# Optimization experiments

Hardware: AMD Instinct MI355X
Metric: run time of the kernel (lower is better)

The kernel has to match this reference:

```python
import jax, jax.numpy as jnp
import numpy as np
import math

B, L, D, H = 4, 2048, 512, 8
DH = D // H
FACTOR = 5.0
EPS = 1e-9
# static top-k count: min(L_q, max(1, int(factor * log(L_q + eps))))
K_TOP = min(L, max(1, int(FACTOR * math.log(L + EPS))))  # = 38
SCALE = 1.0 / math.sqrt(DH)


def setup_inputs() -> dict:
    key = jax.random.key(0)
    ks = jax.random.split(key, 9)
    s = 1.0 / math.sqrt(D)
    return {
        "x": jax.random.normal(ks[0], (B, L, D), jnp.float32),
        "Wq": jax.random.normal(ks[1], (D, D), jnp.float32) * s,
        "bq": jax.random.normal(ks[2], (D,), jnp.float32) * 0.01,
        "Wk": jax.random.normal(ks[3], (D, D), jnp.float32) * s,
        "bk": jax.random.normal(ks[4], (D,), jnp.float32) * 0.01,
        "Wv": jax.random.normal(ks[5], (D, D), jnp.float32) * s,
        "bv": jax.random.normal(ks[6], (D,), jnp.float32) * 0.01,
        "Wo": jax.random.normal(ks[7], (D, D), jnp.float32) * s,
        "bo": jax.random.normal(ks[8], (D,), jnp.float32) * 0.01,
    }


def _project(x, W, b):
    # [B, L, D] -> [B*H, L, DH]
    y = x @ W + b
    return y.reshape(B, L, H, DH).transpose(0, 2, 1, 3).reshape(B * H, L, DH)


def reference(x, Wq, bq, Wk, bk, Wv, bv, Wo, bo):
    Q = _project(x, Wq, bq)
    K = _project(x, Wk, bk)
    V = _project(x, Wv, bv)

    # full scores for sparsity measure: [BH, L, L]
    scores = jnp.einsum('bqd,bkd->bqk', Q, K) * SCALE
    M = scores.max(axis=-1) - scores.mean(axis=-1)  # [BH, L]
    _, top_idx = jax.lax.top_k(M, K_TOP)            # [BH, K_TOP]

    # gather sparse queries, sparse attention
    Q_sparse = jnp.take_along_axis(Q, top_idx[:, :, None], axis=1)  # [BH, K_TOP, DH]
    scores_sparse = jnp.einsum('bqd,bkd->bqk', Q_sparse, K) * SCALE
    attn = jax.nn.softmax(scores_sparse, axis=-1)
    context_sparse = attn @ V                                        # [BH, K_TOP, DH]

    # mean-filled context, scatter sparse results back
    V_mean = V.mean(axis=1, keepdims=True)                           # [BH, 1, DH]
    context = jnp.broadcast_to(V_mean, (B * H, L, DH))
    bidx = jnp.arange(B * H)[:, None]
    context = context.at[bidx, top_idx, :].set(context_sparse)

    # merge heads, output projection
    out = context.reshape(B, H, L, DH).transpose(0, 2, 1, 3).reshape(B, L, D)
    return out @ Wo + bo
```

## Files before the change

### kernel.cpp

```cpp
#include <hip/hip_runtime.h>

#define BB   4
#define LL   2048
#define DD   512
#define HH   8
#define DH   64
#define BH   32
#define KTOP 38
#define NCAND 64
#define SCALEF 0.125f

#define NSP  16
#define CHK  128
#define QPAD 48
#define SCS  132
#define VST  66

typedef __attribute__((ext_vector_type(8))) short bf16x8;
typedef __attribute__((ext_vector_type(8))) unsigned short ushort8;
typedef __attribute__((ext_vector_type(4))) float f32x4;

__device__ __forceinline__ ushort f32_to_bf16_rn(float x) {
    unsigned u = __float_as_uint(x);
    u += 0x7fffu + ((u >> 16) & 1u);
    return (ushort)(u >> 16);
}
__device__ __forceinline__ float bf16_to_f32(ushort h) {
    return __uint_as_float(((unsigned)h) << 16);
}
__device__ __forceinline__ unsigned int pack_hl(float x) {
    ushort h = f32_to_bf16_rn(x);
    ushort l = f32_to_bf16_rn(x - bf16_to_f32(h));
    return ((unsigned int)l << 16) | (unsigned int)h;
}

__global__ __launch_bounds__(256) void split_x(const float* __restrict__ X,
                                               ushort* __restrict__ XH,
                                               ushort* __restrict__ XL) {
    const size_t c = (size_t)blockIdx.x * 256 + threadIdx.x;
    const float4 v = *(const float4*)&X[c * 4];
    ushort4 h, l;
    h.x = f32_to_bf16_rn(v.x); l.x = f32_to_bf16_rn(v.x - bf16_to_f32(h.x));
    h.y = f32_to_bf16_rn(v.y); l.y = f32_to_bf16_rn(v.y - bf16_to_f32(h.y));
    h.z = f32_to_bf16_rn(v.z); l.z = f32_to_bf16_rn(v.z - bf16_to_f32(h.z));
    h.w = f32_to_bf16_rn(v.w); l.w = f32_to_bf16_rn(v.w - bf16_to_f32(h.w));
    *(ushort4*)&XH[c * 4] = h;
    *(ushort4*)&XL[c * 4] = l;
}

__global__ __launch_bounds__(256) void split_wT(const float* __restrict__ W0,
                                                const float* __restrict__ W1,
                                                const float* __restrict__ W2,
                                                const float* __restrict__ W3,
                                                ushort* __restrict__ WTH,
                                                ushort* __restrict__ WTL) {
    __shared__ float tile[32][33];
    const int z = blockIdx.z;
    const float* W = (z == 0) ? W0 : (z == 1) ? W1 : (z == 2) ? W2 : W3;
    ushort* oh = WTH + (size_t)z * DD * DD;
    ushort* ol = WTL + (size_t)z * DD * DD;
    const int n0 = blockIdx.x * 32, k0 = blockIdx.y * 32;
    const int t = threadIdx.x;
    const int r = t >> 5, c = t & 31;
    #pragma unroll
    for (int i = 0; i < 4; i++)
        tile[r + i * 8][c] = W[(size_t)(k0 + r + i * 8) * DD + n0 + c];
    __syncthreads();
    #pragma unroll
    for (int i = 0; i < 4; i++) {
        int row = r + i * 8;
        float v = tile[c][row];
        ushort h = f32_to_bf16_rn(v);
        oh[(size_t)(n0 + row) * DD + k0 + c] = h;
        ol[(size_t)(n0 + row) * DD + k0 + c] = f32_to_bf16_rn(v - bf16_to_f32(h));
    }
}

__global__ __launch_bounds__(256) void mfma_gemm_qkv(const ushort* __restrict__ AH,
                                                     const ushort* __restrict__ AL,
                                                     const ushort* __restrict__ BTH,
                                                     const ushort* __restrict__ BTL,
                                                     const float* __restrict__ bq,
                                                     const float* __restrict__ bk,
                                                     const float* __restrict__ bv,
                                                     float* __restrict__ Qp,
                                                     float* __restrict__ Kp,
                                                     float* __restrict__ Vp,
                                                     ushort* __restrict__ KH) {
    __shared__ ushort BHs[64 * 40];
    __shared__ ushort BLs[64 * 40];

    const int t = threadIdx.x;
    const int w = t >> 6, lane = t & 63;
    const int quad = lane >> 4, n16 = lane & 15;
    const int row0 = blockIdx.y * 128;
    const int n0   = blockIdx.x * 64;
    const int z    = n0 >> 9;
    const int nloc0 = n0 & 511;

    const float* bias = (z == 0) ? bq : (z == 1) ? bk : bv;
    float* Y          = (z == 0) ? Qp : (z == 1) ? Kp : Vp;

    f32x4 acc[2][4] = {};

    size_t arow_off[2];
    #pragma unroll
    for (int mt = 0; mt < 2; mt++)
        arow_off[mt] = (size_t)(row0 + w * 32 + mt * 16 + n16) * DD;

    const int brow = t >> 2, bc8 = t & 3;
    const size_t bbase = (size_t)z * DD * DD;

    for (int k0 = 0; k0 < DD; k0 += 32) {
        {
            const size_t goff = bbase + (size_t)(nloc0 + brow) * DD + k0 + bc8 * 8;
            const uint4 vh = *(const uint4*)&BTH[goff];
            const uint4 vl = *(const uint4*)&BTL[goff];
            *(uint4*)&BHs[brow * 40 + bc8 * 8] = vh;
            *(uint4*)&BLs[brow * 40 + bc8 * 8] = vl;
        }
        bf16x8 ah[2], al[2];
        #pragma unroll
        for (int mt = 0; mt < 2; mt++) {
            size_t off = arow_off[mt] + k0 + quad * 8;
            ah[mt] = *(const bf16x8*)&AH[off];
            al[mt] = *(const bf16x8*)&AL[off];
        }
        __syncthreads();

        bf16x8 bh[4], bl[4];
        #pragma unroll
        for (int nt = 0; nt < 4; nt++) {
            int off = (nt * 16 + n16) * 40 + quad * 8;
            bh[nt] = *(const bf16x8*)&BHs[off];
            bl[nt] = *(const bf16x8*)&BLs[off];
        }
        #pragma unroll
        for (int mt = 0; mt < 2; mt++)
            #pragma unroll
            for (int nt = 0; nt < 4; nt++) {
                acc[mt][nt] = __builtin_amdgcn_mfma_f32_16x16x32_bf16(ah[mt], bh[nt], acc[mt][nt], 0, 0, 0);
                acc[mt][nt] = __builtin_amdgcn_mfma_f32_16x16x32_bf16(ah[mt], bl[nt], acc[mt][nt], 0, 0, 0);
                acc[mt][nt] = __builtin_amdgcn_mfma_f32_16x16x32_bf16(al[mt], bh[nt], acc[mt][nt], 0, 0, 0);
            }
        __syncthreads();
    }

    #pragma unroll
    for (int mt = 0; mt < 2; mt++)
        #pragma unroll
        for (int nt = 0; nt < 4; nt++) {
            const int c = nloc0 + nt * 16 + n16;
            const float bvv = bias[c];
            const int h = c >> 6, dh = c & 63;
            #pragma unroll
            for (int r = 0; r < 4; r++) {
                int R = row0 + w * 32 + mt * 16 + quad * 4 + r;
                int b = R >> 11, l = R & 2047;
                float v = acc[mt][nt][r] + bvv;
                size_t off = (((size_t)(b * HH + h)) * LL + l) * DH + dh;
                Y[off] = v;
                if (z == 1) KH[off] = f32_to_bf16_rn(v);
            }
        }
}

__global__ __launch_bounds__(256) void mfma_gemm_out(const ushort* __restrict__ AH,
                                                     const ushort* __restrict__ AL,
                                                     const ushort* __restrict__ BTH,
                                                     const ushort* __restrict__ BTL,
                                                     const float* __restrict__ bias,
                                                     float* __restrict__ Y) {
    __shared__ ushort BHs[64 * 40];
    __shared__ ushort BLs[64 * 40];

    const int t = threadIdx.x;
    const int w = t >> 6, lane = t & 63;
    const int quad = lane >> 4, n16 = lane & 15;
    const int row0 = blockIdx.y * 128;
    const int n0   = blockIdx.x * 64;

    f32x4 acc[2][4] = {};

    size_t arow_off[2];
    #pragma unroll
    for (int mt = 0; mt < 2; mt++) {
        int R = row0 + w * 32 + mt * 16 + n16;
        int b = R >> 11, l = R & 2047;
        arow_off[mt] = ((size_t)b * HH) * LL * DH + (size_t)l * DH;
    }

    const int brow = t >> 2, bc8 = t & 3;

    for (int k0 = 0; k0 < DD; k0 += 32) {
        {
            const size_t goff = (size_t)(n0 + brow) * DD + k0 + bc8 * 8;
            const uint4 vh = *(const uint4*)&BTH[goff];
            const uint4 vl = *(const uint4*)&BTL[goff];
            *(uint4*)&BHs[brow * 40 + bc8 * 8] = vh;
            *(uint4*)&BLs[brow * 40 + bc8 * 8] = vl;
        }
        bf16x8 ah[2], al[2];
        #pragma unroll
        for (int mt = 0; mt < 2; mt++) {
            int k = k0 + quad * 8;
            int h = k >> 6, dh = k & 63;
            size_t off = arow_off[mt] + (size_t)h * LL * DH + dh;
            ah[mt] = *(const bf16x8*)&AH[off];
            al[mt] = *(const bf16x8*)&AL[off];
        }
        __syncthreads();

        bf16x8 bh[4], bl[4];
        #pragma unroll
        for (int nt = 0; nt < 4; nt++) {
            int off = (nt * 16 + n16) * 40 + quad * 8;
            bh[nt] = *(const bf16x8*)&BHs[off];
            bl[nt] = *(const bf16x8*)&BLs[off];
        }
        #pragma unroll
        for (int mt = 0; mt < 2; mt++)
            #pragma unroll
            for (int nt = 0; nt < 4; nt++) {
                acc[mt][nt] = __builtin_amdgcn_mfma_f32_16x16x32_bf16(ah[mt], bh[nt], acc[mt][nt], 0, 0, 0);
                acc[mt][nt] = __builtin_amdgcn_mfma_f32_16x16x32_bf16(ah[mt], bl[nt], acc[mt][nt], 0, 0, 0);
                acc[mt][nt] = __builtin_amdgcn_mfma_f32_16x16x32_bf16(al[mt], bh[nt], acc[mt][nt], 0, 0, 0);
            }
        __syncthreads();
    }

    #pragma unroll
    for (int mt = 0; mt < 2; mt++)
        #pragma unroll
        for (int nt = 0; nt < 4; nt++) {
            const int c = n0 + nt * 16 + n16;
            const float bvv = bias[c];
            #pragma unroll
            for (int r = 0; r < 4; r++) {
                int R = row0 + w * 32 + mt * 16 + quad * 4 + r;
                Y[(size_t)R * DD + c] = acc[mt][nt][r] + bvv;
            }
        }
}

__global__ __launch_bounds__(256) void mean_partial(const float* __restrict__ Kp,
                                                    const float* __restrict__ Vp,
                                                    float* __restrict__ partial) {
    __shared__ float red[256];
    const int bh = blockIdx.x;
    const int srcI = blockIdx.y;
    const int z  = blockIdx.z;
    const float* src = srcI ? Vp : Kp;
    const int t = threadIdx.x;
    const int d = t & 63, ch = t >> 6;
    const int l0 = z * 128 + ch * 32;
    float s = 0.f;
    for (int l = l0; l < l0 + 32; l++)
        s += src[((size_t)bh * LL + l) * DH + d];
    red[t] = s;
    __syncthreads();
    if (t < 64)
        partial[((size_t)((bh * 2 + srcI) * 16 + z)) * 64 + t] =
            red[t] + red[t + 64] + red[t + 128] + red[t + 192];
}

__global__ __launch_bounds__(64) void mean_reduce(const float* __restrict__ partial,
                                                  float* __restrict__ Kmean,
                                                  float* __restrict__ Vmean) {
    const int bh = blockIdx.x;
    const int srcI = blockIdx.y;
    const int t  = threadIdx.x;
    float s = 0.f;
    #pragma unroll
    for (int z = 0; z < 16; z++)
        s += partial[((size_t)((bh * 2 + srcI) * 16 + z)) * 64 + t];
    float* dst = srcI ? Vmean : Kmean;
    dst[bh * DH + t] = s * (1.0f / LL);
}

__global__ __launch_bounds__(256) void mfma_stats(const float* __restrict__ Qp,
                                                  const ushort* __restrict__ KH,
                                                  const float* __restrict__ Kmean,
                                                  float* __restrict__ MP,
                                                  float* __restrict__ MMD) {
    __shared__ ushort KS[128 * 72];
    __shared__ float  Km[64];

    const int bh = blockIdx.y;
    const int q0 = blockIdx.x * 128;
    const int z  = blockIdx.z;
    const int t    = threadIdx.x;
    const int w    = t >> 6;
    const int lane = t & 63;
    const int quad = lane >> 4;
    const int n16  = lane & 15;

    if (z == 0) {
        if (t < 64) Km[t] = Kmean[bh * DH + t];
        __syncthreads();
        if (t < 128) {
            const float4* qr = (const float4*)&Qp[((size_t)bh * LL + q0 + t) * DH];
            const float4* km4 = (const float4*)Km;
            float md = 0.f;
            #pragma unroll
            for (int i = 0; i < 16; i++) {
                float4 a = qr[i], b = km4[i];
                md += a.x * b.x + a.y * b.y + a.z * b.z + a.w * b.w;
            }
            MMD[(size_t)bh * LL + q0 + t] = SCALEF * md;
        }
    }

    bf16x8 aH[2][2], aL[2][2];
    #pragma unroll
    for (int mt = 0; mt < 2; mt++) {
        const float* qrp = &Qp[((size_t)bh * LL + q0 + w * 32 + mt * 16 + n16) * DH + quad * 8];
        float v[16];
        *(float4*)&v[0]  = *(const float4*)(qrp);
        *(float4*)&v[4]  = *(const float4*)(qrp + 4);
        *(float4*)&v[8]  = *(const float4*)(qrp + 32);
        *(float4*)&v[12] = *(const float4*)(qrp + 36);
        #pragma unroll
        for (int j = 0; j < 8; j++) {
            ushort h0 = f32_to_bf16_rn(v[j]);
            aH[mt][0][j] = (short)h0;
            aL[mt][0][j] = (short)f32_to_bf16_rn(v[j] - bf16_to_f32(h0));
            ushort h1 = f32_to_bf16_rn(v[8 + j]);
            aH[mt][1][j] = (short)h1;
            aL[mt][1][j] = (short)f32_to_bf16_rn(v[8 + j] - bf16_to_f32(h1));
        }
    }

    f32x4 maxv[2] = {{-3.4e38f, -3.4e38f, -3.4e38f, -3.4e38f},
                     {-3.4e38f, -3.4e38f, -3.4e38f, -3.4e38f}};

    const int kbase = z * (LL / 2);
    for (int kt0 = kbase; kt0 < kbase + LL / 2; kt0 += 128) {
        __syncthreads();
        #pragma unroll
        for (int i = 0; i < 4; i++) {
            int f = i * 256 + t;
            int row = f >> 3, c8 = f & 7;
            const uint4 v = *(const uint4*)&KH[((size_t)(bh * LL + kt0 + row)) * DH + c8 * 8];
            *(uint4*)&KS[row * 72 + c8 * 8] = v;
        }
        __syncthreads();

        for (int ktl = 0; ktl < 128; ktl += 16) {
            const ushort* bp = &KS[(size_t)(ktl + n16) * 72 + quad * 8];
            bf16x8 bH0 = *(const bf16x8*)(bp);
            bf16x8 bH1 = *(const bf16x8*)(bp + 32);
            #pragma unroll
            for (int mt = 0; mt < 2; mt++) {
                f32x4 acc = {0.f, 0.f, 0.f, 0.f};
                acc = __builtin_amdgcn_mfma_f32_16x16x32_bf16(aH[mt][0], bH0, acc, 0, 0, 0);
                acc = __builtin_amdgcn_mfma_f32_16x16x32_bf16(aH[mt][1], bH1, acc, 0, 0, 0);
                acc = __builtin_amdgcn_mfma_f32_16x16x32_bf16(aL[mt][0], bH0, acc, 0, 0, 0);
                acc = __builtin_amdgcn_mfma_f32_16x16x32_bf16(aL[mt][1], bH1, acc, 0, 0, 0);
                maxv[mt][0] = fmaxf(maxv[mt][0], acc[0]);
                maxv[mt][1] = fmaxf(maxv[mt][1], acc[1]);
                maxv[mt][2] = fmaxf(maxv[mt][2], acc[2]);
                maxv[mt][3] = fmaxf(maxv[mt][3], acc[3]);
            }
        }
    }

    #pragma unroll
    for (int off = 1; off < 16; off <<= 1)
        #pragma unroll
        for (int mt = 0; mt < 2; mt++)
            #pragma unroll
            for (int r = 0; r < 4; r++)
                maxv[mt][r] = fmaxf(maxv[mt][r], __shfl_xor(maxv[mt][r], off));

    if (n16 == 0) {
        #pragma unroll
        for (int mt = 0; mt < 2; mt++)
            #pragma unroll
            for (int r = 0; r < 4; r++) {
                int lq = w * 32 + mt * 16 + quad * 4 + r;
                MP[((size_t)z * BH + bh) * LL + q0 + lq] = SCALEF * maxv[mt][r];
            }
    }
}

__global__ __launch_bounds__(256) void topk_radix(const float* __restrict__ MP,
                                                  const float* __restrict__ MMD,
                                                  int* __restrict__ out_idx) {
    __shared__ unsigned hist[4096];
    __shared__ unsigned segc[256];
    __shared__ unsigned suf[256];
    __shared__ int sb1, sc1, sb2;
    __shared__ int ncnt;
    const int bh = blockIdx.x;
    const int t  = threadIdx.x;

    unsigned key[8];
    #pragma unroll
    for (int i = 0; i < 8; i++) {
        size_t q = (size_t)i * 256 + t;
        float v = fmaxf(MP[(size_t)bh * LL + q], MP[((size_t)BH + bh) * LL + q])
                  - MMD[(size_t)bh * LL + q];
        unsigned u = __float_as_uint(v);
        key[i] = (u & 0x80000000u) ? ~u : (u | 0x80000000u);
    }

    #pragma unroll
    for (int i = 0; i < 16; i++) hist[t * 16 + i] = 0;
    if (t == 0) ncnt = 0;
    __syncthreads();
    #pragma unroll
    for (int i = 0; i < 8; i++) atomicAdd(&hist[key[i] >> 20], 1u);
    __syncthreads();
    unsigned s = 0;
    #pragma unroll
    for (int i = 0; i < 16; i++) s += hist[t * 16 + i];
    segc[t] = s;
    __syncthreads();
    if (t == 0) {
        unsigned run = 0;
        for (int i = 255; i >= 0; i--) { suf[i] = run; run += segc[i]; }
    }
    __syncthreads();
    if (suf[t] < NCAND && suf[t] + segc[t] >= NCAND) {
        unsigned c = suf[t];
        for (int j = 15; j >= 0; j--) {
            int b = t * 16 + j;
            if (c + hist[b] >= NCAND) { sb1 = b; sc1 = (int)c; break; }
            c += hist[b];
        }
    }
    __syncthreads();
    const unsigned b1 = (unsigned)sb1;
    const int c1 = sc1;

    #pragma unroll
    for (int i = 0; i < 16; i++) hist[t * 16 + i] = 0;
    __syncthreads();
    #pragma unroll
    for (int i = 0; i < 8; i++)
        if ((key[i] >> 20) == b1) atomicAdd(&hist[(key[i] >> 8) & 0xfffu], 1u);
    __syncthreads();
    s = 0;
    #pragma unroll
    for (int i = 0; i < 16; i++) s += hist[t * 16 + i];
    segc[t] = s;
    __syncthreads();
    if (t == 0) {
        unsigned run = 0;
        for (int i = 255; i >= 0; i--) { suf[i] = run; run += segc[i]; }
    }
    __syncthreads();
    const int need2 = NCAND - c1;
    if ((int)suf[t] < need2 && (int)(suf[t] + segc[t]) >= need2) {
        unsigned c = suf[t];
        for (int j = 15; j >= 0; j--) {
            int b = t * 16 + j;
            if ((int)(c + hist[b]) >= need2) { sb2 = b; break; }
            c += hist[b];
        }
    }
    __syncthreads();
    const unsigned b2 = (unsigned)sb2;

    #pragma unroll
    for (int i = 0; i < 8; i++)
        if ((key[i] >> 20) > b1) {
            int p = atomicAdd(&ncnt, 1);
            out_idx[bh * NCAND + p] = i * 256 + t;
        }
    __syncthreads();
    #pragma unroll
    for (int i = 0; i < 8; i++)
        if ((key[i] >> 20) == b1 && ((key[i] >> 8) & 0xfffu) > b2) {
            int p = atomicAdd(&ncnt, 1);
            out_idx[bh * NCAND + p] = i * 256 + t;
        }
    __syncthreads();
    #pragma unroll
    for (int i = 0; i < 8; i++)
        if ((key[i] >> 20) == b1 && ((key[i] >> 8) & 0xfffu) == b2) {
            int p = atomicAdd(&ncnt, 1);
            if (p < NCAND) out_idx[bh * NCAND + p] = i * 256 + t;
        }
}

__global__ __launch_bounds__(256) void exact_partial(const float* __restrict__ Qp,
                                                     const float* __restrict__ Kp,
                                                     const int* __restrict__ CAND,
                                                     float* __restrict__ EMP) {
    __shared__ float Qs[64][65];
    __shared__ float Ks[64][65];
    __shared__ int   cidx[64];
    const int bh = blockIdx.y;
    const int chunk = blockIdx.x;
    const int t = threadIdx.x;
    const int tx = t & 15, ty = t >> 4;

    if (t < 64) cidx[t] = CAND[bh * NCAND + t];
    __syncthreads();
    #pragma unroll
    for (int i = 0; i < 4; i++) {
        int f = i * 256 + t;
        int row = f >> 4, c4 = f & 15;
        const float4 v = *(const float4*)&Qp[((size_t)bh * LL + cidx[row]) * DH + c4 * 4];
        *(float4*)&Qs[row][c4 * 4] = v;
    }

    float mx[4] = {-3.4e38f, -3.4e38f, -3.4e38f, -3.4e38f};

    for (int kt = 0; kt < 4; kt++) {
        __syncthreads();
        #pragma unroll
        for (int i = 0; i < 4; i++) {
            int f = i * 256 + t;
            int row = f >> 4, c4 = f & 15;
            const float4 v = *(const float4*)&Kp[((size_t)(bh * LL + chunk * 256 + kt * 64 + row)) * DH + c4 * 4];
            *(float4*)&Ks[row][c4 * 4] = v;
        }
        __syncthreads();
        float acc[4][4] = {};
        #pragma unroll 8
        for (int dd = 0; dd < 64; dd++) {
            float a[4], b[4];
            #pragma unroll
            for (int i = 0; i < 4; i++) a[i] = Qs[ty * 4 + i][dd];
            #pragma unroll
            for (int j = 0; j < 4; j++) b[j] = Ks[tx * 4 + j][dd];
            #pragma unroll
            for (int i = 0; i < 4; i++)
                #pragma unroll
                for (int j = 0; j < 4; j++) acc[i][j] += a[i] * b[j];
        }
        #pragma unroll
        for (int i = 0; i < 4; i++)
            #pragma unroll
            for (int j = 0; j < 4; j++) mx[i] = fmaxf(mx[i], acc[i][j]);
    }

    #pragma unroll
    for (int off = 1; off < 16; off <<= 1)
        #pragma unroll
        for (int i = 0; i < 4; i++)
            mx[i] = fmaxf(mx[i], __shfl_xor(mx[i], off));

    if (tx == 0) {
        #pragma unroll
        for (int i = 0; i < 4; i++)
            EMP[((size_t)bh * NCAND + ty * 4 + i) * 8 + chunk] = mx[i];
    }
}

__global__ __launch_bounds__(64) void select_kernel(const float* __restrict__ EMP,
                                                    const int* __restrict__ CAND,
                                                    const float* __restrict__ Qp,
                                                    const float* __restrict__ Kmean,
                                                    int* __restrict__ TIDX) {
    __shared__ float Km[64];
    const int bh = blockIdx.x;
    const int t  = threadIdx.x;
    Km[t] = Kmean[bh * DH + t];
    __syncthreads();

    const int qi = CAND[bh * NCAND + t];
    float mx = -3.4e38f;
    #pragma unroll
    for (int c = 0; c < 8; c++) mx = fmaxf(mx, EMP[((size_t)bh * NCAND + t) * 8 + c]);

    const float4* qr = (const float4*)&Qp[((size_t)bh * LL + qi) * DH];
    const float4* km4 = (const float4*)Km;
    float md = 0.f;
    #pragma unroll
    for (int i = 0; i < 16; i++) {
        float4 a = qr[i], b = km4[i];
        md += a.x * b.x + a.y * b.y + a.z * b.z + a.w * b.w;
    }
    float v = SCALEF * mx - SCALEF * md;

    for (int it = 0; it < KTOP; it++) {
        float bv = v; int bq = qi;
        #pragma unroll
        for (int off = 1; off < 64; off <<= 1) {
            float ov = __shfl_xor(bv, off);
            int   oq = __shfl_xor(bq, off);
            if (ov > bv || (ov == bv && oq < bq)) { bv = ov; bq = oq; }
        }
        if (t == 0) TIDX[bh * KTOP + it] = bq;
        if (qi == bq) v = -3.4e38f;
    }
}

__global__ __launch_bounds__(256) void fill_kernel(const float* __restrict__ Vmean,
                                                   ushort* __restrict__ CH,
                                                   ushort* __restrict__ CL) {
    const size_t c = (size_t)blockIdx.x * 256 + threadIdx.x;
    const int d4 = (int)(c & 15) * 4;
    const int bh = (int)(c >> 15);
    const float4 v = *(const float4*)&Vmean[bh * DH + d4];
    ushort4 h, l;
    h.x = f32_to_bf16_rn(v.x); l.x = f32_to_bf16_rn(v.x - bf16_to_f32(h.x));
    h.y = f32_to_bf16_rn(v.y); l.y = f32_to_bf16_rn(v.y - bf16_to_f32(h.y));
    h.z = f32_to_bf16_rn(v.z); l.z = f32_to_bf16_rn(v.z - bf16_to_f32(h.z));
    h.w = f32_to_bf16_rn(v.w); l.w = f32_to_bf16_rn(v.w - bf16_to_f32(h.w));
    *(ushort4*)&CH[c * 4] = h;
    *(ushort4*)&CL[c * 4] = l;
}

__global__ __launch_bounds__(256) void sparse_partial(const float* __restrict__ Qp,
                                                      const ushort* __restrict__ KH,
                                                      const float* __restrict__ Vp,
                                                      const int* __restrict__ TIDX,
                                                      float* __restrict__ OPART,
                                                      float* __restrict__ MPART,
                                                      float* __restrict__ LPART) {
    __shared__ float sc[QPAD * SCS];
    __shared__ unsigned int Vhl[CHK * VST];
    const int bh = blockIdx.y;
    const int ck = blockIdx.x;
    const int k0 = ck * CHK;
    const int t = threadIdx.x;
    const int w = t >> 6, lane = t & 63;
    const int quad = lane >> 4, n16 = lane & 15;
    const int mt = w;

    #pragma unroll
    for (int i = 0; i < 8; i++) {
        int e = i * 256 + t;
        int key = e >> 4, c4 = e & 15;
        const float4 v = *(const float4*)&Vp[((size_t)(bh * LL + k0 + key)) * DH + c4 * 4];
        uint4 p;
        p.x = pack_hl(v.x); p.y = pack_hl(v.y);
        p.z = pack_hl(v.z); p.w = pack_hl(v.w);
        *(uint4*)&Vhl[key * VST + c4 * 4] = p;
    }

    if (mt < 3) {
        bf16x8 aH[2], aL[2];
        {
            int q = mt * 16 + n16;
            int qq = q < KTOP ? q : (KTOP - 1);
            const float* qp = &Qp[((size_t)bh * LL + TIDX[bh * KTOP + qq]) * DH];
            #pragma unroll
            for (int kf = 0; kf < 2; kf++) {
                float v[8];
                *(float4*)&v[0] = *(const float4*)(qp + kf * 32 + quad * 8);
                *(float4*)&v[4] = *(const float4*)(qp + kf * 32 + quad * 8 + 4);
                #pragma unroll
                for (int j = 0; j < 8; j++) {
                    ushort h = f32_to_bf16_rn(v[j]);
                    aH[kf][j] = (short)h;
                    aL[kf][j] = (short)f32_to_bf16_rn(v[j] - bf16_to_f32(h));
                }
            }
        }
        #pragma unroll
        for (int nt = 0; nt < 8; nt++) {
            f32x4 acc = {0.f, 0.f, 0.f, 0.f};
            #pragma unroll
            for (int kf = 0; kf < 2; kf++) {
                bf16x8 b = *(const bf16x8*)&KH[((size_t)(bh * LL + k0 + nt * 16 + n16)) * DH + kf * 32 + quad * 8];
                acc = __builtin_amdgcn_mfma_f32_16x16x32_bf16(aH[kf], b, acc, 0, 0, 0);
                acc = __builtin_amdgcn_mfma_f32_16x16x32_bf16(aL[kf], b, acc, 0, 0, 0);
            }
            #pragma unroll
            for (int r = 0; r < 4; r++)
                sc[(mt * 16 + quad * 4 + r) * SCS + nt * 16 + n16] = acc[r];
        }
    }
    __syncthreads();

    for (int row = w; row < KTOP; row += 4) {
        float v0 = sc[row * SCS + lane];
        float v1 = sc[row * SCS + 64 + lane];
        float m = fmaxf(v0, v1);
        #pragma unroll
        for (int off = 1; off < 64; off <<= 1)
            m = fmaxf(m, __shfl_xor(m, off));
        const float ms = m * SCALEF;
        float e0 = __expf(v0 * SCALEF - ms);
        float e1 = __expf(v1 * SCALEF - ms);
        float l = e0 + e1;
        #pragma unroll
        for (int off = 1; off < 64; off <<= 1)
            l += __shfl_xor(l, off);
        sc[row * SCS + lane]      = e0;
        sc[row * SCS + 64 + lane] = e1;
        if (lane == 0) {
            MPART[((size_t)ck * BH + bh) * KTOP + row] = ms;
            LPART[((size_t)ck * BH + bh) * KTOP + row] = l;
        }
    }
    __syncthreads();

    if (mt < 3) {
        f32x4 acc[4] = {};
        #pragma unroll
        for (int kf = 0; kf < 4; kf++) {
            bf16x8 ph, pl;
            {
                const float* pp = &sc[(mt * 16 + n16) * SCS + kf * 32 + quad * 8];
                float v[8];
                *(float4*)&v[0] = *(const float4*)(pp);
                *(float4*)&v[4] = *(const float4*)(pp + 4);
                #pragma unroll
                for (int j = 0; j < 8; j++) {
                    ushort h = f32_to_bf16_rn(v[j]);
                    ph[j] = (short)h;
                    pl[j] = (short)f32_to_bf16_rn(v[j] - bf16_to_f32(h));
                }
            }
            #pragma unroll
            for (int nt = 0; nt < 4; nt++) {
                unsigned int u[8];
                #pragma unroll
                for (int j = 0; j < 8; j++)
                    u[j] = Vhl[(kf * 32 + quad * 8 + j) * VST + nt * 16 + n16];
                bf16x8 vh, vl;
                #pragma unroll
                for (int j = 0; j < 8; j++) {
                    vh[j] = (short)(u[j] & 0xffffu);
                    vl[j] = (short)(u[j] >> 16);
                }
                acc[nt] = __builtin_amdgcn_mfma_f32_16x16x32_bf16(ph, vh, acc[nt], 0, 0, 0);
                acc[nt] = __builtin_amdgcn_mfma_f32_16x16x32_bf16(ph, vl, acc[nt], 0, 0, 0);
                acc[nt] = __builtin_amdgcn_mfma_f32_16x16x32_bf16(pl, vh, acc[nt], 0, 0, 0);
            }
        }
        #pragma unroll
        for (int nt = 0; nt < 4; nt++)
            #pragma unroll
            for (int r = 0; r < 4; r++) {
                int q = mt * 16 + quad * 4 + r;
                if (q < KTOP)
                    OPART[(((size_t)ck * BH + bh) * KTOP + q) * DH + nt * 16 + n16] = acc[nt][r];
            }
    }
}

__global__ __launch_bounds__(256) void sparse_combine(const float* __restrict__ OPART,
                                                      const float* __restrict__ MPART,
                                                      const float* __restrict__ LPART,
                                                      const int* __restrict__ TIDX,
                                                      ushort* __restrict__ CH,
                                                      ushort* __restrict__ CL) {
    __shared__ float wts[NSP][KTOP];
    __shared__ float inv[KTOP];
    __shared__ int   tq[KTOP];
    const int bh = blockIdx.x;
    const int t  = threadIdx.x;
    if (t < KTOP) {
        float m[NSP];
        float mx = -3.4e38f;
        #pragma unroll
        for (int c = 0; c < NSP; c++) {
            m[c] = MPART[((size_t)c * BH + bh) * KTOP + t];
            mx = fmaxf(mx, m[c]);
        }
        float L = 0.f;
        #pragma unroll
        for (int c = 0; c < NSP; c++) {
            float wc = __expf(m[c] - mx);
            wts[c][t] = wc;
            L += wc * LPART[((size_t)c * BH + bh) * KTOP + t];
        }
        inv[t] = 1.0f / L;
        tq[t] = TIDX[bh * KTOP + t];
    }
    __syncthreads();
    for (int i = 0; i < 10; i++) {
        int idx = i * 256 + t;
        if (idx >= KTOP * DH) break;
        int q = idx >> 6, d = idx & 63;
        float o = 0.f;
        #pragma unroll
        for (int c = 0; c < NSP; c++)
            o += wts[c][q] * OPART[(((size_t)c * BH + bh) * KTOP + q) * DH + d];
        float val = o * inv[q];
        size_t off = ((size_t)bh * LL + tq[q]) * DH + d;
        ushort h = f32_to_bf16_rn(val);
        CH[off] = h;
        CL[off] = f32_to_bf16_rn(val - bf16_to_f32(h));
    }
}

extern "C" void kernel_launch(void* const* d_in, const int* in_sizes, int n_in,
                              void* d_out, int out_size, void* d_ws, size_t ws_size,
                              hipStream_t stream) {
    const float* x  = (const float*)d_in[0];
    const float* Wq = (const float*)d_in[1];
    const float* bq = (const float*)d_in[2];
    const float* Wk = (const float*)d_in[3];
    const float* bk = (const float*)d_in[4];
    const float* Wv = (const float*)d_in[5];
    const float* bv = (const float*)d_in[6];
    const float* Wo = (const float*)d_in[7];
    const float* bo = (const float*)d_in[8];
    float* out = (float*)d_out;

    float* ws = (float*)d_ws;
    const size_t QSZ = (size_t)BH * LL * DH;
    float* Qp    = ws;
    float* Kp    = ws + QSZ;
    float* Vp    = ws + 2 * QSZ;
    float* MMD   = ws + 3 * QSZ;
    float* KMEAN = MMD + (size_t)BH * LL;
    float* VMEAN = KMEAN + BH * DH;
    int*   CAND  = (int*)(VMEAN + BH * DH);
    int*   TIDX  = CAND + BH * NCAND;
    float* EMP   = (float*)(TIDX + BH * KTOP);
    float* MEANP = EMP + (size_t)BH * NCAND * 8;
    float* MP    = MEANP + 65536;
    ushort* WTH  = (ushort*)(ws + 3 * QSZ + 524288);
    ushort* WTL  = WTH + (size_t)4 * DD * DD;
    ushort* XH   = WTL + (size_t)4 * DD * DD;
    ushort* XL   = XH + QSZ;
    ushort* CH   = XH;
    ushort* CL   = XL;
    ushort* KH   = XL + QSZ;
    float* OPART = (float*)(KH + QSZ);
    float* MPART = OPART + (size_t)NSP * BH * KTOP * DH;
    float* LPART = MPART + (size_t)NSP * BH * KTOP;
    const size_t WOFF = (size_t)DD * DD;

    split_wT<<<dim3(16, 16, 4), 256, 0, stream>>>(Wq, Wk, Wv, Wo, WTH, WTL);
    split_x<<<(int)(QSZ / 1024), 256, 0, stream>>>(x, XH, XL);

    mfma_gemm_qkv<<<dim3(24, 64), 256, 0, stream>>>(XH, XL, WTH, WTL,
                                                    bq, bk, bv, Qp, Kp, Vp, KH);

    mean_partial<<<dim3(BH, 2, 16), 256, 0, stream>>>(Kp, Vp, MEANP);
    mean_reduce<<<dim3(BH, 2), 64, 0, stream>>>(MEANP, KMEAN, VMEAN);

    mfma_stats<<<dim3(16, BH, 2), 256, 0, stream>>>(Qp, KH, KMEAN, MP, MMD);

    topk_radix<<<BH, 256, 0, stream>>>(MP, MMD, CAND);

    exact_partial<<<dim3(8, BH), 256, 0, stream>>>(Qp, Kp, CAND, EMP);

    select_kernel<<<BH, 64, 0, stream>>>(EMP, CAND, Qp, KMEAN, TIDX);

    fill_kernel<<<(int)(QSZ / 1024), 256, 0, stream>>>(VMEAN, CH, CL);

    sparse_partial<<<dim3(NSP, BH), 256, 0, stream>>>(Qp, KH, Vp, TIDX, OPART, MPART, LPART);
    sparse_combine<<<BH, 256, 0, stream>>>(OPART, MPART, LPART, TIDX, CH, CL);

    mfma_gemm_out<<<dim3(8, 64), 256, 0, stream>>>(CH, CL, WTH + 3 * WOFF, WTL + 3 * WOFF, bo, out);
}
```

Before: 301.5 us.

## Replace dense output projection with mean-context base plus sparse scatter corrections

Uses linearity of the output projection. Since most context rows equal the per-head V mean, each batch gets one base row (Vmean·Wo + bo), which is broadcast to every output row. Sparse rows then add (context − Vmean)·Wo_h through atomics. This removes the fill kernel, the Wo split and the full 8192x512x512 output GEMM. The QKV GEMM k-step is also widened to 64 with a larger LDS tile. Atomic accumulation makes summation order nondeterministic, and the base_kernel GEMV runs on only 4 blocks.

```diff
diff --git a/kernel.cpp b/kernel.cpp
--- a/kernel.cpp
+++ b/kernel.cpp
@@ -51,12 +51,11 @@
 __global__ __launch_bounds__(256) void split_wT(const float* __restrict__ W0,
                                                 const float* __restrict__ W1,
                                                 const float* __restrict__ W2,
-                                                const float* __restrict__ W3,
                                                 ushort* __restrict__ WTH,
                                                 ushort* __restrict__ WTL) {
     __shared__ float tile[32][33];
     const int z = blockIdx.z;
-    const float* W = (z == 0) ? W0 : (z == 1) ? W1 : (z == 2) ? W2 : W3;
+    const float* W = (z == 0) ? W0 : (z == 1) ? W1 : W2;
     ushort* oh = WTH + (size_t)z * DD * DD;
     ushort* ol = WTL + (size_t)z * DD * DD;
     const int n0 = blockIdx.x * 32, k0 = blockIdx.y * 32;
@@ -87,8 +86,8 @@
                                                      float* __restrict__ Kp,
                                                      float* __restrict__ Vp,
                                                      ushort* __restrict__ KH) {
-    __shared__ ushort BHs[64 * 40];
-    __shared__ ushort BLs[64 * 40];
+    __shared__ ushort BHs[64 * 72];
+    __shared__ ushort BLs[64 * 72];
 
     const int t = threadIdx.x;
     const int w = t >> 6, lane = t & 63;
@@ -108,40 +107,41 @@
     for (int mt = 0; mt < 2; mt++)
         arow_off[mt] = (size_t)(row0 + w * 32 + mt * 16 + n16) * DD;
 
-    const int brow = t >> 2, bc8 = t & 3;
     const size_t bbase = (size_t)z * DD * DD;
 
-    for (int k0 = 0; k0 < DD; k0 += 32) {
-        {
-            const size_t goff = bbase + (size_t)(nloc0 + brow) * DD + k0 + bc8 * 8;
-            const uint4 vh = *(const uint4*)&BTH[goff];
-            const uint4 vl = *(const uint4*)&BTL[goff];
-            *(uint4*)&BHs[brow * 40 + bc8 * 8] = vh;
-            *(uint4*)&BLs[brow * 40 + bc8 * 8] = vl;
-        }
-        bf16x8 ah[2], al[2];
-        #pragma unroll
-        for (int mt = 0; mt < 2; mt++) {
-            size_t off = arow_off[mt] + k0 + quad * 8;
-            ah[mt] = *(const bf16x8*)&AH[off];
-            al[mt] = *(const bf16x8*)&AL[off];
-        }
+    for (int k0 = 0; k0 < DD; k0 += 64) {
+        #pragma unroll
+        for (int i = 0; i < 2; i++) {
+            int s = i * 256 + t;
+            int row = s >> 3, c8 = s & 7;
+            const size_t goff = bbase + (size_t)(nloc0 + row) * DD + k0 + c8 * 8;
+            *(uint4*)&BHs[row * 72 + c8 * 8] = *(const uint4*)&BTH[goff];
+            *(uint4*)&BLs[row * 72 + c8 * 8] = *(const uint4*)&BTL[goff];
+        }
+        bf16x8 ah[2][2], al[2][2];
+        #pragma unroll
+        for (int mt = 0; mt < 2; mt++)
+            #pragma unroll
+            for (int kf = 0; kf < 2; kf++) {
+                size_t off = arow_off[mt] + k0 + kf * 32 + quad * 8;
+                ah[mt][kf] = *(const bf16x8*)&AH[off];
+                al[mt][kf] = *(const bf16x8*)&AL[off];
+            }
         __syncthreads();
 
-        bf16x8 bh[4], bl[4];
-        #pragma unroll
-        for (int nt = 0; nt < 4; nt++) {
-            int off = (nt * 16 + n16) * 40 + quad * 8;
-            bh[nt] = *(const bf16x8*)&BHs[off];
-            bl[nt] = *(const bf16x8*)&BLs[off];
-        }
-        #pragma unroll
-        for (int mt = 0; mt < 2; mt++)
+        #pragma unroll
+        for (int kf = 0; kf < 2; kf++)
             #pragma unroll
             for (int nt = 0; nt < 4; nt++) {
-                acc[mt][nt] = __builtin_amdgcn_mfma_f32_16x16x32_bf16(ah[mt], bh[nt], acc[mt][nt], 0, 0, 0);
-                acc[mt][nt] = __builtin_amdgcn_mfma_f32_16x16x32_bf16(ah[mt], bl[nt], acc[mt][nt], 0, 0, 0);
-                acc[mt][nt] = __builtin_amdgcn_mfma_f32_16x16x32_bf16(al[mt], bh[nt], acc[mt][nt], 0, 0, 0);
+                int boff = (nt * 16 + n16) * 72 + kf * 32 + quad * 8;
+                bf16x8 bh = *(const bf16x8*)&BHs[boff];
+                bf16x8 bl = *(const bf16x8*)&BLs[boff];
+                #pragma unroll
+                for (int mt = 0; mt < 2; mt++) {
+                    acc[mt][nt] = __builtin_amdgcn_mfma_f32_16x16x32_bf16(ah[mt][kf], bh, acc[mt][nt], 0, 0, 0);
+                    acc[mt][nt] = __builtin_amdgcn_mfma_f32_16x16x32_bf16(ah[mt][kf], bl, acc[mt][nt], 0, 0, 0);
+                    acc[mt][nt] = __builtin_amdgcn_mfma_f32_16x16x32_bf16(al[mt][kf], bh, acc[mt][nt], 0, 0, 0);
+                }
             }
         __syncthreads();
     }
@@ -161,84 +161,6 @@
                 size_t off = (((size_t)(b * HH + h)) * LL + l) * DH + dh;
                 Y[off] = v;
                 if (z == 1) KH[off] = f32_to_bf16_rn(v);
-            }
-        }
-}
-
-__global__ __launch_bounds__(256) void mfma_gemm_out(const ushort* __restrict__ AH,
-                                                     const ushort* __restrict__ AL,
-                                                     const ushort* __restrict__ BTH,
-                                                     const ushort* __restrict__ BTL,
-                                                     const float* __restrict__ bias,
-                                                     float* __restrict__ Y) {
-    __shared__ ushort BHs[64 * 40];
-    __shared__ ushort BLs[64 * 40];
-
-    const int t = threadIdx.x;
-    const int w = t >> 6, lane = t & 63;
-    const int quad = lane >> 4, n16 = lane & 15;
-    const int row0 = blockIdx.y * 128;
-    const int n0   = blockIdx.x * 64;
-
-    f32x4 acc[2][4] = {};
-
-    size_t arow_off[2];
-    #pragma unroll
-    for (int mt = 0; mt < 2; mt++) {
-        int R = row0 + w * 32 + mt * 16 + n16;
-        int b = R >> 11, l = R & 2047;
-        arow_off[mt] = ((size_t)b * HH) * LL * DH + (size_t)l * DH;
-    }
-
-    const int brow = t >> 2, bc8 = t & 3;
-
-    for (int k0 = 0; k0 < DD; k0 += 32) {
-        {
-            const size_t goff = (size_t)(n0 + brow) * DD + k0 + bc8 * 8;
-            const uint4 vh = *(const uint4*)&BTH[goff];
-            const uint4 vl = *(const uint4*)&BTL[goff];
-            *(uint4*)&BHs[brow * 40 + bc8 * 8] = vh;
-            *(uint4*)&BLs[brow * 40 + bc8 * 8] = vl;
-        }
-        bf16x8 ah[2], al[2];
-        #pragma unroll
-        for (int mt = 0; mt < 2; mt++) {
-            int k = k0 + quad * 8;
-            int h = k >> 6, dh = k & 63;
-            size_t off = arow_off[mt] + (size_t)h * LL * DH + dh;
-            ah[mt] = *(const bf16x8*)&AH[off];
-            al[mt] = *(const bf16x8*)&AL[off];
-        }
-        __syncthreads();
-
-        bf16x8 bh[4], bl[4];
-        #pragma unroll
-        for (int nt = 0; nt < 4; nt++) {
-            int off = (nt * 16 + n16) * 40 + quad * 8;
-            bh[nt] = *(const bf16x8*)&BHs[off];
-            bl[nt] = *(const bf16x8*)&BLs[off];
-        }
-        #pragma unroll
-        for (int mt = 0; mt < 2; mt++)
-            #pragma unroll
-            for (int nt = 0; nt < 4; nt++) {
-                acc[mt][nt] = __builtin_amdgcn_mfma_f32_16x16x32_bf16(ah[mt], bh[nt], acc[mt][nt], 0, 0, 0);
-                acc[mt][nt] = __builtin_amdgcn_mfma_f32_16x16x32_bf16(ah[mt], bl[nt], acc[mt][nt], 0, 0, 0);
-                acc[mt][nt] = __builtin_amdgcn_mfma_f32_16x16x32_bf16(al[mt], bh[nt], acc[mt][nt], 0, 0, 0);
-            }
-        __syncthreads();
-    }
-
-    #pragma unroll
-    for (int mt = 0; mt < 2; mt++)
-        #pragma unroll
-        for (int nt = 0; nt < 4; nt++) {
-            const int c = n0 + nt * 16 + n16;
-            const float bvv = bias[c];
-            #pragma unroll
-            for (int r = 0; r < 4; r++) {
-                int R = row0 + w * 32 + mt * 16 + quad * 4 + r;
-                Y[(size_t)R * DD + c] = acc[mt][nt][r] + bvv;
             }
         }
 }
@@ -278,6 +200,54 @@
     dst[bh * DH + t] = s * (1.0f / LL);
 }
 
+__global__ __launch_bounds__(256) void base_kernel(const float* __restrict__ Vmean,
+                                                   const float* __restrict__ Wo,
+                                                   const float* __restrict__ bo,
+                                                   float* __restrict__ BASE) {
+    __shared__ float vm[512];
+    const int b = blockIdx.x;
+    const int t = threadIdx.x;
+    vm[t]       = Vmean[b * 512 + t];
+    vm[t + 256] = Vmean[b * 512 + t + 256];
+    __syncthreads();
+    #pragma unroll
+    for (int cc = 0; cc < 2; cc++) {
+        const int c = cc * 256 + t;
+        float s = 0.f;
+        for (int k = 0; k < 512; k++) s += vm[k] * Wo[(size_t)k * 512 + c];
+        BASE[b * 512 + c] = s + bo[c];
+    }
+}
+
+__global__ __launch_bounds__(256) void broadcast_base(const float* __restrict__ BASE,
+                                                      float* __restrict__ out) {
+    const size_t f = ((size_t)blockIdx.x * 256 + threadIdx.x) * 4;
+    const int b = (int)(f >> 20);
+    const int c = (int)(f & 511);
+    *(float4*)&out[f] = *(const float4*)&BASE[b * 512 + c];
+}
+
+__global__ __launch_bounds__(256) void scatter_kernel(const float* __restrict__ CORR,
+                                                      const int* __restrict__ TIDX,
+                                                      const float* __restrict__ Wo,
+                                                      float* __restrict__ out) {
+    __shared__ float cr[64];
+    const int q = blockIdx.x, bh = blockIdx.y;
+    const int b = bh >> 3, h = bh & 7;
+    const int t = threadIdx.x;
+    if (t < 64) cr[t] = CORR[((size_t)bh * KTOP + q) * DH + t];
+    __syncthreads();
+    const int l = TIDX[bh * KTOP + q];
+    #pragma unroll
+    for (int cc = 0; cc < 2; cc++) {
+        const int c = cc * 256 + t;
+        float s = 0.f;
+        #pragma unroll
+        for (int d = 0; d < 64; d++) s += cr[d] * Wo[(size_t)(h * 64 + d) * 512 + c];
+        atomicAdd(&out[((size_t)b * LL + l) * DD + c], s);
+    }
+}
+
 __global__ __launch_bounds__(256) void mfma_stats(const float* __restrict__ Qp,
                                                   const ushort* __restrict__ KH,
                                                   const float* __restrict__ Kmean,
@@ -588,22 +558,6 @@
         if (t == 0) TIDX[bh * KTOP + it] = bq;
         if (qi == bq) v = -3.4e38f;
     }
-}
-
-__global__ __launch_bounds__(256) void fill_kernel(const float* __restrict__ Vmean,
-                                                   ushort* __restrict__ CH,
-                                                   ushort* __restrict__ CL) {
-    const size_t c = (size_t)blockIdx.x * 256 + threadIdx.x;
-    const int d4 = (int)(c & 15) * 4;
-    const int bh = (int)(c >> 15);
-    const float4 v = *(const float4*)&Vmean[bh * DH + d4];
-    ushort4 h, l;
-    h.x = f32_to_bf16_rn(v.x); l.x = f32_to_bf16_rn(v.x - bf16_to_f32(h.x));
-    h.y = f32_to_bf16_rn(v.y); l.y = f32_to_bf16_rn(v.y - bf16_to_f32(h.y));
-    h.z = f32_to_bf16_rn(v.z); l.z = f32_to_bf16_rn(v.z - bf16_to_f32(h.z));
-    h.w = f32_to_bf16_rn(v.w); l.w = f32_to_bf16_rn(v.w - bf16_to_f32(h.w));
-    *(ushort4*)&CH[c * 4] = h;
-    *(ushort4*)&CL[c * 4] = l;
 }
 
 __global__ __launch_bounds__(256) void sparse_partial(const float* __restrict__ Qp,
@@ -740,12 +694,10 @@
 __global__ __launch_bounds__(256) void sparse_combine(const float* __restrict__ OPART,
                                                       const float* __restrict__ MPART,
                                                       const float* __restrict__ LPART,
-                                                      const int* __restrict__ TIDX,
-                                                      ushort* __restrict__ CH,
-                                                      ushort* __restrict__ CL) {
+                                                      const float* __restrict__ Vmean,
+                                                      float* __restrict__ CORR) {
     __shared__ float wts[NSP][KTOP];
     __shared__ float inv[KTOP];
-    __shared__ int   tq[KTOP];
     const int bh = blockIdx.x;
     const int t  = threadIdx.x;
     if (t < KTOP) {
@@ -764,7 +716,6 @@
             L += wc * LPART[((size_t)c * BH + bh) * KTOP + t];
         }
         inv[t] = 1.0f / L;
-        tq[t] = TIDX[bh * KTOP + t];
     }
     __syncthreads();
     for (int i = 0; i < 10; i++) {
@@ -775,11 +726,7 @@
         #pragma unroll
         for (int c = 0; c < NSP; c++)
             o += wts[c][q] * OPART[(((size_t)c * BH + bh) * KTOP + q) * DH + d];
-        float val = o * inv[q];
-        size_t off = ((size_t)bh * LL + tq[q]) * DH + d;
-        ushort h = f32_to_bf16_rn(val);
-        CH[off] = h;
-        CL[off] = f32_to_bf16_rn(val - bf16_to_f32(h));
+        CORR[((size_t)bh * KTOP + q) * DH + d] = o * inv[q] - Vmean[bh * DH + d];
     }
 }
 
@@ -810,19 +757,18 @@
     float* EMP   = (float*)(TIDX + BH * KTOP);
     float* MEANP = EMP + (size_t)BH * NCAND * 8;
     float* MP    = MEANP + 65536;
-    ushort* WTH  = (ushort*)(ws + 3 * QSZ + 524288);
-    ushort* WTL  = WTH + (size_t)4 * DD * DD;
-    ushort* XH   = WTL + (size_t)4 * DD * DD;
+    float* CORR  = MP + (size_t)2 * BH * LL;
+    float* BASE  = CORR + (size_t)BH * KTOP * DH;
+    ushort* WTH  = (ushort*)(ws + 3 * QSZ + 786432);
+    ushort* WTL  = WTH + (size_t)3 * DD * DD;
+    ushort* XH   = WTL + (size_t)3 * DD * DD;
     ushort* XL   = XH + QSZ;
-    ushort* CH   = XH;
-    ushort* CL   = XL;
     ushort* KH   = XL + QSZ;
     float* OPART = (float*)(KH + QSZ);
     float* MPART = OPART + (size_t)NSP * BH * KTOP * DH;
     float* LPART = MPART + (size_t)NSP * BH * KTOP;
-    const size_t WOFF = (size_t)DD * DD;
-
-    split_wT<<<dim3(16, 16, 4), 256, 0, stream>>>(Wq, Wk, Wv, Wo, WTH, WTL);
+
+    split_wT<<<dim3(16, 16, 3), 256, 0, stream>>>(Wq, Wk, Wv, WTH, WTL);
     split_x<<<(int)(QSZ / 1024), 256, 0, stream>>>(x, XH, XL);
 
     mfma_gemm_qkv<<<dim3(24, 64), 256, 0, stream>>>(XH, XL, WTH, WTL,
@@ -831,6 +777,9 @@
     mean_partial<<<dim3(BH, 2, 16), 256, 0, stream>>>(Kp, Vp, MEANP);
     mean_reduce<<<dim3(BH, 2), 64, 0, stream>>>(MEANP, KMEAN, VMEAN);
 
+    base_kernel<<<BB, 256, 0, stream>>>(VMEAN, Wo, bo, BASE);
+    broadcast_base<<<(int)(QSZ / 1024), 256, 0, stream>>>(BASE, out);
+
     mfma_stats<<<dim3(16, BH, 2), 256, 0, stream>>>(Qp, KH, KMEAN, MP, MMD);
 
     topk_radix<<<BH, 256, 0, stream>>>(MP, MMD, CAND);
@@ -839,10 +788,8 @@
 
     select_kernel<<<BH, 64, 0, stream>>>(EMP, CAND, Qp, KMEAN, TIDX);
 
-    fill_kernel<<<(int)(QSZ / 1024), 256, 0, stream>>>(VMEAN, CH, CL);
-
     sparse_partial<<<dim3(NSP, BH), 256, 0, stream>>>(Qp, KH, Vp, TIDX, OPART, MPART, LPART);
-    sparse_combine<<<BH, 256, 0, stream>>>(OPART, MPART, LPART, TIDX, CH, CL);
-
-    mfma_gemm_out<<<dim3(8, 64), 256, 0, stream>>>(CH, CL, WTH + 3 * WOFF, WTL + 3 * WOFF, bo, out);
-}
+    sparse_combine<<<BH, 256, 0, stream>>>(OPART, MPART, LPART, VMEAN, CORR);
+
+    scatter_kernel<<<dim3(KTOP, BH), 256, 0, stream>>>(CORR, TIDX, Wo, out);
+}
```

New measurement: 312.1 us. 3.5% more time.
